# Kernel optimization log

Measured on AMD Instinct MI355X. Metric: run time of the kernel, lower is better.

Reference implementation:

```python
import jax, jax.numpy as jnp
import numpy as np

B, C, G, K, S, P, R = 4, 256, 16, 7, 1, 3, 4
H = W = 56


def setup_inputs() -> dict:
    key = jax.random.key(0)
    k1, k2, k3 = jax.random.split(key, 3)
    x = jax.random.normal(k1, (B, C, H, W), jnp.float32)
    reduce_w = jax.random.normal(k2, (C // R, C), jnp.float32) * 0.05
    reduce_b = jnp.zeros((C // R,), jnp.float32)
    span_w = jax.random.normal(k3, (K * K * G, C // R), jnp.float32) * 0.05
    span_b = jnp.zeros((K * K * G,), jnp.float32)
    return {"x": x, "reduce_w": reduce_w, "reduce_b": reduce_b,
            "span_w": span_w, "span_b": span_b}


def reference(x, reduce_w, reduce_b, span_w, span_b):
    b, c, h_in, w_in = x.shape
    Ho = (h_in + 2 * P - K) // S + 1
    Wo = (w_in + 2 * P - K) // S + 1
    # im2col patches, channel ordering (C, kh, kw) — matches torch.nn.Unfold
    patches = jax.lax.conv_general_dilated_patches(
        x, (K, K), (S, S), [(P, P), (P, P)])  # (B, C*K*K, Ho, Wo)
    patches = patches.reshape(b, G, c // G, K * K, Ho, Wo)
    # kernel generation branch: AvgPool(s) (identity for s=1) -> 1x1 reduce -> 1x1 span
    if S > 1:
        xk = jax.lax.reduce_window(x, 0.0, jax.lax.add,
                                   (1, 1, S, S), (1, 1, S, S), 'VALID') / (S * S)
    else:
        xk = x
    h = jnp.einsum('bchw,oc->bohw', xk, reduce_w) + reduce_b[None, :, None, None]
    kern = jnp.einsum('bchw,oc->bohw', h, span_w) + span_b[None, :, None, None]
    kern = kern.reshape(b, G, 1, K * K, Ho, Wo)
    # dynamic per-pixel depthwise-style multiply-reduce over the K*K window
    out = (kern * patches).sum(axis=3)  # (B, G, C//G, Ho, Wo)
    return out.reshape(b, c, Ho, Wo)
```

## Files before the change

### kernel.cpp

```cpp
#include <hip/hip_runtime.h>
#include <stdint.h>

#define HH   56
#define WW   56
#define HWP  (HH * WW)
#define CC   256
#define GG   16
#define CGR  16
#define KT   7
#define KK   49
#define RCP  32
#define TH   2
#define XP   548
#define RP   68
#define TP   116

typedef _Float16 h2_t __attribute__((ext_vector_type(2)));
typedef _Float16 v8h  __attribute__((ext_vector_type(8)));
typedef float    v4f  __attribute__((ext_vector_type(4)));
union pk32 { uint32_t u; h2_t h; };
union frag { uint32_t u[4]; v8h h; };

__global__ __launch_bounds__(256)
void pack_weights(const float* __restrict__ sw, const float* __restrict__ rw,
                  uint32_t* __restrict__ sw2, uint32_t* __restrict__ rw2)
{
    const int id = blockIdx.x * 256 + threadIdx.x;
    if (id < 25088) {
        pk32 p; p.h = h2_t{(_Float16)sw[2 * id], (_Float16)sw[2 * id + 1]};
        sw2[id] = p.u;
    } else {
        const int j = id - 25088;
        pk32 p; p.h = h2_t{(_Float16)rw[2 * j], (_Float16)rw[2 * j + 1]};
        rw2[j] = p.u;
    }
}

__global__ __launch_bounds__(256)
void gemm1_mfma(const uint32_t* __restrict__ rw2, const float* __restrict__ rb,
                const float* __restrict__ x, uint32_t* __restrict__ h2)
{
    const int b   = blockIdx.z;
    const int px0 = blockIdx.x * 32;
    const int t = threadIdx.x;
    const int wave = t >> 6, lane = t & 63, quad = lane >> 4, n16 = lane & 15;

    __shared__ __align__(16) uint32_t ldsB[2][32][36];

    const int c2l = t >> 3;
    const int px4 = t & 7;
    const float* xb = x + (size_t)b * CC * HWP + px0 + 4 * px4;

    v4f acc[2];
    acc[0] = v4f{0.f,0.f,0.f,0.f}; acc[1] = v4f{0.f,0.f,0.f,0.f};

    {
        const int c = 2 * c2l;
        const float4 a  = *(const float4*)&xb[(size_t)c * HWP];
        const float4 bb = *(const float4*)&xb[(size_t)(c + 1) * HWP];
        pk32 u0,u1,u2,u3;
        u0.h = h2_t{(_Float16)a.x, (_Float16)bb.x};
        u1.h = h2_t{(_Float16)a.y, (_Float16)bb.y};
        u2.h = h2_t{(_Float16)a.z, (_Float16)bb.z};
        u3.h = h2_t{(_Float16)a.w, (_Float16)bb.w};
        uint4 w; w.x=u0.u; w.y=u1.u; w.z=u2.u; w.w=u3.u;
        *(uint4*)&ldsB[0][c2l][4 * px4] = w;
    }
    __syncthreads();

    const uint32_t* rwm = rw2 + (size_t)(wave * 16 + n16) * 128;
#pragma unroll
    for (int k = 0; k < 4; ++k) {
        if (k < 3) {
            const int c = (k + 1) * 64 + 2 * c2l;
            const float4 a  = *(const float4*)&xb[(size_t)c * HWP];
            const float4 bb = *(const float4*)&xb[(size_t)(c + 1) * HWP];
            pk32 u0,u1,u2,u3;
            u0.h = h2_t{(_Float16)a.x, (_Float16)bb.x};
            u1.h = h2_t{(_Float16)a.y, (_Float16)bb.y};
            u2.h = h2_t{(_Float16)a.z, (_Float16)bb.z};
            u3.h = h2_t{(_Float16)a.w, (_Float16)bb.w};
            uint4 w; w.x=u0.u; w.y=u1.u; w.z=u2.u; w.w=u3.u;
            *(uint4*)&ldsB[(k + 1) & 1][c2l][4 * px4] = w;
        }
        frag a0, a1;
        *(uint4*)a0.u = *(const uint4*)&rwm[k * 32 + quad * 4];
        *(uint4*)a1.u = *(const uint4*)&rwm[k * 32 + 16 + quad * 4];
        const uint32_t (*B)[36] = ldsB[k & 1];
#pragma unroll
        for (int nt = 0; nt < 2; ++nt) {
            frag b0, b1;
#pragma unroll
            for (int jj = 0; jj < 4; ++jj) {
                b0.u[jj] = B[quad * 4 + jj][nt * 16 + n16];
                b1.u[jj] = B[16 + quad * 4 + jj][nt * 16 + n16];
            }
            acc[nt] = __builtin_amdgcn_mfma_f32_16x16x32_f16(a0.h, b0.h, acc[nt], 0, 0, 0);
            acc[nt] = __builtin_amdgcn_mfma_f32_16x16x32_f16(a1.h, b1.h, acc[nt], 0, 0, 0);
        }
        __syncthreads();
    }
    uint32_t* hb = h2 + (size_t)b * RCP * HWP + px0;
#pragma unroll
    for (int nt = 0; nt < 2; ++nt) {
#pragma unroll
        for (int pr = 0; pr < 2; ++pr) {
            const int m0 = wave * 16 + quad * 4 + 2 * pr;
            pk32 q;
            q.h = h2_t{(_Float16)(acc[nt][2 * pr] + rb[m0]),
                       (_Float16)(acc[nt][2 * pr + 1] + rb[m0 + 1])};
            hb[(size_t)(wave * 8 + quad * 2 + pr) * HWP + nt * 16 + n16] = q.u;
        }
    }
}

__global__ __launch_bounds__(256, 2)
void invol_fused(const float* __restrict__ x, const uint32_t* __restrict__ h2,
                 const uint32_t* __restrict__ sw2, const float* __restrict__ sb,
                 float* __restrict__ out)
{
    const int h0 = blockIdx.x * TH;
    const int g  = blockIdx.y;
    const int b  = blockIdx.z;

    __shared__ __align__(16) float    sX[16 * XP];
    __shared__ __align__(16) uint32_t ldsT[32 * TP];
    __shared__ __align__(16) float    sK[KK * 112];
    const int t = threadIdx.x;
    const int wave = t >> 6, lane = t & 63, quad = lane >> 4, n16 = lane & 15;

    const int mt0 = wave * 16 + n16;
    const int mtap = mt0 > 48 ? 48 : mt0;
    const uint32_t* swr = sw2 + ((size_t)g * KK + mtap) * RCP + quad * 4;
    frag a0, a1;
    *(uint4*)a0.u = *(const uint4*)swr;
    *(uint4*)a1.u = *(const uint4*)(swr + 16);

    float bvv[4];
#pragma unroll
    for (int reg = 0; reg < 4; ++reg) {
        const int tp = wave * 16 + quad * 4 + reg;
        bvv[reg] = (tp < KK) ? sb[g * KK + tp] : 0.f;
    }

    {
        const uint32_t* hb = h2 + (size_t)b * RCP * HWP + h0 * WW;
#pragma unroll
        for (int k = 0; k < 14; ++k) {
            const int i = t + 256 * k;
            const int px = i % 112, c2 = i / 112;
            ldsT[c2 * TP + px] = hb[(size_t)c2 * HWP + px];
        }
    }

    {
        const int hc = t & 1, rr = (t >> 1) & 7, ch = t >> 4;
        *(float4*)&sX[ch * XP + rr * RP + (hc ? 60 : 0)] = make_float4(0,0,0,0);
    }

    {
        const float* xb = x + (size_t)(b * CC + g * CGR) * HWP;
#pragma unroll
        for (int k = 0; k < 7; ++k) {
            const int i = t + 256 * k;
            const int w4 = i % 14, rr = (i / 14) % 8, ch = i / 112;
            const int hh = h0 - 3 + rr;
            float4 v = make_float4(0,0,0,0);
            if (hh >= 0 && hh < HH)
                v = *(const float4*)&xb[(size_t)ch * HWP + hh * WW + 4 * w4];
            *(float4*)&sX[ch * XP + rr * RP + 4 + 4 * w4] = v;
        }
    }
    __syncthreads();

    v4f acc[7];
#pragma unroll
    for (int nt = 0; nt < 7; ++nt) acc[nt] = v4f{0.f,0.f,0.f,0.f};
#pragma unroll
    for (int nt = 0; nt < 7; ++nt) {
        const int px = nt * 16 + n16;
        frag b0, b1;
#pragma unroll
        for (int jj = 0; jj < 4; ++jj) {
            b0.u[jj] = ldsT[(quad * 4 + jj) * TP + px];
            b1.u[jj] = ldsT[(16 + quad * 4 + jj) * TP + px];
        }
        acc[nt] = __builtin_amdgcn_mfma_f32_16x16x32_f16(a0.h, b0.h, acc[nt], 0, 0, 0);
        acc[nt] = __builtin_amdgcn_mfma_f32_16x16x32_f16(a1.h, b1.h, acc[nt], 0, 0, 0);
    }
#pragma unroll
    for (int nt = 0; nt < 7; ++nt) {
        const int px = nt * 16 + n16;
#pragma unroll
        for (int reg = 0; reg < 4; ++reg) {
            const int tp = wave * 16 + quad * 4 + reg;
            if (tp < KK) sK[tp * 112 + px] = acc[nt][reg] + bvv[reg];
        }
    }
    __syncthreads();

    if (t < 224) {
        const int ch = t & 15;
        const int q  = t >> 4;
        const int r  = q & 1;
        const int wq = q >> 1;
        const float* xc = sX + ch * XP;
        float* op = out + (size_t)(b * CC + g * CGR + ch) * HWP + (h0 + r) * WW;
#pragma unroll
        for (int wb = 0; wb < 2; ++wb) {
            const int w0 = 4 * wq + 28 * wb;
            float o0=0.f, o1=0.f, o2=0.f, o3=0.f;
#pragma unroll
            for (int kh = 0; kh < KT; ++kh) {
                const int rr = r + kh;
                const float* xr = xc + rr * RP + w0;
                float xf[12];
                *(float4*)&xf[0] = *(const float4*)&xr[0];
                *(float4*)&xf[4] = *(const float4*)&xr[4];
                *(float4*)&xf[8] = *(const float4*)&xr[8];
                const float* kp = sK + (kh * KT) * 112 + r * WW + w0;
#pragma unroll
                for (int kw = 0; kw < KT; ++kw) {
                    const float4 kf = *(const float4*)&kp[kw * 112];
                    o0 += kf.x * xf[kw + 1];
                    o1 += kf.y * xf[kw + 2];
                    o2 += kf.z * xf[kw + 3];
                    o3 += kf.w * xf[kw + 4];
                }
            }
            *(float4*)&op[w0] = make_float4(o0, o1, o2, o3);
        }
    }
}

extern "C" void kernel_launch(void* const* d_in, const int* in_sizes, int n_in,
                              void* d_out, int out_size, void* d_ws, size_t ws_size,
                              hipStream_t stream)
{
    const float* x  = (const float*)d_in[0];
    const float* rw = (const float*)d_in[1];
    const float* rb = (const float*)d_in[2];
    const float* sw = (const float*)d_in[3];
    const float* sb = (const float*)d_in[4];
    float* out  = (float*)d_out;

    uint32_t* h2  = (uint32_t*)d_ws;
    uint32_t* sw2 = h2 + 4 * RCP * HWP;
    uint32_t* rw2 = sw2 + 25088;

    pack_weights<<<dim3(130, 1, 1), 256, 0, stream>>>(sw, rw, sw2, rw2);
    gemm1_mfma<<<dim3(HWP / 32, 1, 4), 256, 0, stream>>>(rw2, rb, x, h2);
    invol_fused<<<dim3(HH / TH, GG, 4), 256, 0, stream>>>(x, h2, sw2, sb, out);
}
```

Before: 109.9 us.

## Convert involution inner loop to packed fp16 FMA with half-precision LDS tiles

Stores the x tile and the generated per-pixel kernels in LDS as fp16 instead of fp32, and computes the 7x7 multiply-reduce with packed __hfma2 ops, accumulating each kernel row in fp16 before adding it to fp32 totals. LDS buffers are reused and shrunk, and launch bounds are raised to allow more resident blocks per CU. The h2 tile and gemm1 B operand are rearranged so MFMA fragments load as single 128-bit reads, and all fp32-to-fp16 conversions use pkrtz. The main cost targeted is LDS footprint, LDS traffic and FMA count in the main loop; the risk is lower accuracy from fp16 partial sums and round-toward-zero conversion.

Result: faster. 96.14 us (-12.5%).

```diff
diff --git a/kernel.cpp b/kernel.cpp
--- a/kernel.cpp
+++ b/kernel.cpp
@@ -1,9 +1,10 @@
 #include <hip/hip_runtime.h>
+#include <hip/hip_fp16.h>
 #include <stdint.h>
 
 #define HH   56
 #define WW   56
-#define HWP  (HH * WW)
+#define HWP  3136
 #define CC   256
 #define GG   16
 #define CGR  16
@@ -11,90 +12,78 @@
 #define KK   49
 #define RCP  32
 #define TH   2
-#define XP   548
-#define RP   68
-#define TP   116
-
-typedef _Float16 h2_t __attribute__((ext_vector_type(2)));
+#define XROW 32
+#define XPL  260
+
+typedef _Float16 h2_t  __attribute__((ext_vector_type(2)));
+typedef __fp16   fp16x2 __attribute__((ext_vector_type(2)));
 typedef _Float16 v8h  __attribute__((ext_vector_type(8)));
 typedef float    v4f  __attribute__((ext_vector_type(4)));
-union pk32 { uint32_t u; h2_t h; };
+union pk32 { uint32_t u; h2_t h; __half2 hh; fp16x2 f; };
 union frag { uint32_t u[4]; v8h h; };
+
+static __device__ __forceinline__ uint32_t pkrtz(float a, float b) {
+    pk32 p; p.f = __builtin_amdgcn_cvt_pkrtz(a, b); return p.u;
+}
 
 __global__ __launch_bounds__(256)
 void pack_weights(const float* __restrict__ sw, const float* __restrict__ rw,
                   uint32_t* __restrict__ sw2, uint32_t* __restrict__ rw2)
 {
     const int id = blockIdx.x * 256 + threadIdx.x;
-    if (id < 25088) {
-        pk32 p; p.h = h2_t{(_Float16)sw[2 * id], (_Float16)sw[2 * id + 1]};
-        sw2[id] = p.u;
-    } else {
-        const int j = id - 25088;
-        pk32 p; p.h = h2_t{(_Float16)rw[2 * j], (_Float16)rw[2 * j + 1]};
-        rw2[j] = p.u;
-    }
+    if (id < 25088) sw2[id] = pkrtz(sw[2 * id], sw[2 * id + 1]);
+    else            rw2[id - 25088] = pkrtz(rw[2 * (id - 25088)], rw[2 * (id - 25088) + 1]);
 }
 
 __global__ __launch_bounds__(256)
 void gemm1_mfma(const uint32_t* __restrict__ rw2, const float* __restrict__ rb,
                 const float* __restrict__ x, uint32_t* __restrict__ h2)
 {
-    const int b   = blockIdx.z;
-    const int px0 = blockIdx.x * 32;
+    const int b = blockIdx.z, px0 = blockIdx.x * 32;
     const int t = threadIdx.x;
     const int wave = t >> 6, lane = t & 63, quad = lane >> 4, n16 = lane & 15;
 
-    __shared__ __align__(16) uint32_t ldsB[2][32][36];
-
-    const int c2l = t >> 3;
-    const int px4 = t & 7;
-    const float* xb = x + (size_t)b * CC * HWP + px0 + 4 * px4;
+    __shared__ __align__(16) uint32_t ldsB[2][8 * 128];
+
+    const int px = t & 31;
+    const int q4 = t >> 5;
+    const float* xb = x + (size_t)b * CC * HWP + px0 + px;
+
+    float r[4][8];
+#pragma unroll
+    for (int k = 0; k < 4; ++k)
+#pragma unroll
+        for (int cc = 0; cc < 8; ++cc)
+            r[k][cc] = xb[(size_t)(k * 64 + q4 * 8 + cc) * HWP];
+
+    {
+        uint4 w;
+        w.x = pkrtz(r[0][0], r[0][1]); w.y = pkrtz(r[0][2], r[0][3]);
+        w.z = pkrtz(r[0][4], r[0][5]); w.w = pkrtz(r[0][6], r[0][7]);
+        *(uint4*)&ldsB[0][q4 * 128 + px * 4] = w;
+    }
+    __syncthreads();
 
     v4f acc[2];
     acc[0] = v4f{0.f,0.f,0.f,0.f}; acc[1] = v4f{0.f,0.f,0.f,0.f};
-
-    {
-        const int c = 2 * c2l;
-        const float4 a  = *(const float4*)&xb[(size_t)c * HWP];
-        const float4 bb = *(const float4*)&xb[(size_t)(c + 1) * HWP];
-        pk32 u0,u1,u2,u3;
-        u0.h = h2_t{(_Float16)a.x, (_Float16)bb.x};
-        u1.h = h2_t{(_Float16)a.y, (_Float16)bb.y};
-        u2.h = h2_t{(_Float16)a.z, (_Float16)bb.z};
-        u3.h = h2_t{(_Float16)a.w, (_Float16)bb.w};
-        uint4 w; w.x=u0.u; w.y=u1.u; w.z=u2.u; w.w=u3.u;
-        *(uint4*)&ldsB[0][c2l][4 * px4] = w;
-    }
-    __syncthreads();
-
     const uint32_t* rwm = rw2 + (size_t)(wave * 16 + n16) * 128;
 #pragma unroll
     for (int k = 0; k < 4; ++k) {
         if (k < 3) {
-            const int c = (k + 1) * 64 + 2 * c2l;
-            const float4 a  = *(const float4*)&xb[(size_t)c * HWP];
-            const float4 bb = *(const float4*)&xb[(size_t)(c + 1) * HWP];
-            pk32 u0,u1,u2,u3;
-            u0.h = h2_t{(_Float16)a.x, (_Float16)bb.x};
-            u1.h = h2_t{(_Float16)a.y, (_Float16)bb.y};
-            u2.h = h2_t{(_Float16)a.z, (_Float16)bb.z};
-            u3.h = h2_t{(_Float16)a.w, (_Float16)bb.w};
-            uint4 w; w.x=u0.u; w.y=u1.u; w.z=u2.u; w.w=u3.u;
-            *(uint4*)&ldsB[(k + 1) & 1][c2l][4 * px4] = w;
+            uint4 w;
+            w.x = pkrtz(r[k+1][0], r[k+1][1]); w.y = pkrtz(r[k+1][2], r[k+1][3]);
+            w.z = pkrtz(r[k+1][4], r[k+1][5]); w.w = pkrtz(r[k+1][6], r[k+1][7]);
+            *(uint4*)&ldsB[(k + 1) & 1][q4 * 128 + px * 4] = w;
         }
         frag a0, a1;
         *(uint4*)a0.u = *(const uint4*)&rwm[k * 32 + quad * 4];
         *(uint4*)a1.u = *(const uint4*)&rwm[k * 32 + 16 + quad * 4];
-        const uint32_t (*B)[36] = ldsB[k & 1];
+        const uint32_t* B = ldsB[k & 1];
 #pragma unroll
         for (int nt = 0; nt < 2; ++nt) {
             frag b0, b1;
-#pragma unroll
-            for (int jj = 0; jj < 4; ++jj) {
-                b0.u[jj] = B[quad * 4 + jj][nt * 16 + n16];
-                b1.u[jj] = B[16 + quad * 4 + jj][nt * 16 + n16];
-            }
+            *(uint4*)b0.u = *(const uint4*)&B[quad * 128 + (nt * 16 + n16) * 4];
+            *(uint4*)b1.u = *(const uint4*)&B[(4 + quad) * 128 + (nt * 16 + n16) * 4];
             acc[nt] = __builtin_amdgcn_mfma_f32_16x16x32_f16(a0.h, b0.h, acc[nt], 0, 0, 0);
             acc[nt] = __builtin_amdgcn_mfma_f32_16x16x32_f16(a1.h, b1.h, acc[nt], 0, 0, 0);
         }
@@ -102,30 +91,25 @@
     }
     uint32_t* hb = h2 + (size_t)b * RCP * HWP + px0;
 #pragma unroll
-    for (int nt = 0; nt < 2; ++nt) {
+    for (int nt = 0; nt < 2; ++nt)
 #pragma unroll
         for (int pr = 0; pr < 2; ++pr) {
             const int m0 = wave * 16 + quad * 4 + 2 * pr;
-            pk32 q;
-            q.h = h2_t{(_Float16)(acc[nt][2 * pr] + rb[m0]),
-                       (_Float16)(acc[nt][2 * pr + 1] + rb[m0 + 1])};
-            hb[(size_t)(wave * 8 + quad * 2 + pr) * HWP + nt * 16 + n16] = q.u;
-        }
-    }
-}
-
-__global__ __launch_bounds__(256, 2)
+            hb[(size_t)(wave * 8 + quad * 2 + pr) * HWP + nt * 16 + n16] =
+                pkrtz(acc[nt][2 * pr] + rb[m0], acc[nt][2 * pr + 1] + rb[m0 + 1]);
+        }
+}
+
+__global__ __launch_bounds__(256, 4)
 void invol_fused(const float* __restrict__ x, const uint32_t* __restrict__ h2,
                  const uint32_t* __restrict__ sw2, const float* __restrict__ sb,
                  float* __restrict__ out)
 {
-    const int h0 = blockIdx.x * TH;
-    const int g  = blockIdx.y;
-    const int b  = blockIdx.z;
-
-    __shared__ __align__(16) float    sX[16 * XP];
-    __shared__ __align__(16) uint32_t ldsT[32 * TP];
-    __shared__ __align__(16) float    sK[KK * 112];
+    const int h0 = blockIdx.x * TH, g = blockIdx.y, b = blockIdx.z;
+
+    __shared__ __align__(16) uint32_t sXh[16 * XPL];
+    __shared__ __align__(16) uint32_t U[8 * 448];
+
     const int t = threadIdx.x;
     const int wave = t >> 6, lane = t & 63, quad = lane >> 4, n16 = lane & 15;
 
@@ -146,16 +130,24 @@
     {
         const uint32_t* hb = h2 + (size_t)b * RCP * HWP + h0 * WW;
 #pragma unroll
-        for (int k = 0; k < 14; ++k) {
+        for (int k = 0; k < 4; ++k) {
             const int i = t + 256 * k;
-            const int px = i % 112, c2 = i / 112;
-            ldsT[c2 * TP + px] = hb[(size_t)c2 * HWP + px];
-        }
-    }
-
-    {
-        const int hc = t & 1, rr = (t >> 1) & 7, ch = t >> 4;
-        *(float4*)&sX[ch * XP + rr * RP + (hc ? 60 : 0)] = make_float4(0,0,0,0);
+            if (i < 896) {
+                const int px = i % 112, q4 = i / 112;
+                uint4 w;
+                w.x = hb[(size_t)(q4 * 4 + 0) * HWP + px];
+                w.y = hb[(size_t)(q4 * 4 + 1) * HWP + px];
+                w.z = hb[(size_t)(q4 * 4 + 2) * HWP + px];
+                w.w = hb[(size_t)(q4 * 4 + 3) * HWP + px];
+                *(uint4*)&U[q4 * 448 + px * 4] = w;
+            }
+        }
+    }
+
+    {
+        const int ch = t >> 4, rr = (t >> 1) & 7, side = t & 1;
+        uint2 z; z.x = 0; z.y = 0;
+        *(uint2*)&sXh[ch * XPL + rr * XROW + (side ? 30 : 0)] = z;
     }
 
     {
@@ -165,10 +157,11 @@
             const int i = t + 256 * k;
             const int w4 = i % 14, rr = (i / 14) % 8, ch = i / 112;
             const int hh = h0 - 3 + rr;
-            float4 v = make_float4(0,0,0,0);
+            float4 v = make_float4(0.f, 0.f, 0.f, 0.f);
             if (hh >= 0 && hh < HH)
                 v = *(const float4*)&xb[(size_t)ch * HWP + hh * WW + 4 * w4];
-            *(float4*)&sX[ch * XP + rr * RP + 4 + 4 * w4] = v;
+            uint2 p; p.x = pkrtz(v.x, v.y); p.y = pkrtz(v.z, v.w);
+            *(uint2*)&sXh[ch * XPL + rr * XROW + 2 + 2 * w4] = p;
         }
     }
     __syncthreads();
@@ -178,58 +171,70 @@
     for (int nt = 0; nt < 7; ++nt) acc[nt] = v4f{0.f,0.f,0.f,0.f};
 #pragma unroll
     for (int nt = 0; nt < 7; ++nt) {
-        const int px = nt * 16 + n16;
+        const int pxm = (nt * 16 + n16) * 4;
         frag b0, b1;
-#pragma unroll
-        for (int jj = 0; jj < 4; ++jj) {
-            b0.u[jj] = ldsT[(quad * 4 + jj) * TP + px];
-            b1.u[jj] = ldsT[(16 + quad * 4 + jj) * TP + px];
-        }
+        *(uint4*)b0.u = *(const uint4*)&U[quad * 448 + pxm];
+        *(uint4*)b1.u = *(const uint4*)&U[(4 + quad) * 448 + pxm];
         acc[nt] = __builtin_amdgcn_mfma_f32_16x16x32_f16(a0.h, b0.h, acc[nt], 0, 0, 0);
         acc[nt] = __builtin_amdgcn_mfma_f32_16x16x32_f16(a1.h, b1.h, acc[nt], 0, 0, 0);
     }
-#pragma unroll
-    for (int nt = 0; nt < 7; ++nt) {
-        const int px = nt * 16 + n16;
-#pragma unroll
-        for (int reg = 0; reg < 4; ++reg) {
-            const int tp = wave * 16 + quad * 4 + reg;
-            if (tp < KK) sK[tp * 112 + px] = acc[nt][reg] + bvv[reg];
+    __syncthreads();
+
+    {
+        _Float16* sK = (_Float16*)U;
+#pragma unroll
+        for (int nt = 0; nt < 7; ++nt) {
+            const int px = nt * 16 + n16;
+#pragma unroll
+            for (int reg = 0; reg < 4; ++reg) {
+                const int tp = wave * 16 + quad * 4 + reg;
+                if (tp < KK) sK[tp * 112 + px] = (_Float16)(acc[nt][reg] + bvv[reg]);
+            }
         }
     }
     __syncthreads();
 
     if (t < 224) {
-        const int ch = t & 15;
-        const int q  = t >> 4;
-        const int r  = q & 1;
-        const int wq = q >> 1;
-        const float* xc = sX + ch * XP;
-        float* op = out + (size_t)(b * CC + g * CGR + ch) * HWP + (h0 + r) * WW;
-#pragma unroll
-        for (int wb = 0; wb < 2; ++wb) {
-            const int w0 = 4 * wq + 28 * wb;
-            float o0=0.f, o1=0.f, o2=0.f, o3=0.f;
-#pragma unroll
-            for (int kh = 0; kh < KT; ++kh) {
-                const int rr = r + kh;
-                const float* xr = xc + rr * RP + w0;
-                float xf[12];
-                *(float4*)&xf[0] = *(const float4*)&xr[0];
-                *(float4*)&xf[4] = *(const float4*)&xr[4];
-                *(float4*)&xf[8] = *(const float4*)&xr[8];
-                const float* kp = sK + (kh * KT) * 112 + r * WW + w0;
-#pragma unroll
-                for (int kw = 0; kw < KT; ++kw) {
-                    const float4 kf = *(const float4*)&kp[kw * 112];
-                    o0 += kf.x * xf[kw + 1];
-                    o1 += kf.y * xf[kw + 2];
-                    o2 += kf.z * xf[kw + 3];
-                    o3 += kf.w * xf[kw + 4];
+        const int ch = t & 15, q = t >> 4, r = q & 1, wq = q >> 1;
+        const uint32_t* xpl = &sXh[ch * XPL + 4 * wq];
+        float o0=0,o1=0,o2=0,o3=0,o4=0,o5=0,o6=0,o7=0;
+#pragma unroll
+        for (int kh = 0; kh < KT; ++kh) {
+            const int rr = r + kh;
+            uint32_t E[8];
+            *(uint4*)&E[0] = *(const uint4*)&xpl[rr * XROW];
+            *(uint4*)&E[4] = *(const uint4*)&xpl[rr * XROW + 4];
+            uint32_t O[7];
+#pragma unroll
+            for (int j = 0; j < 7; ++j) O[j] = __builtin_amdgcn_alignbit(E[j + 1], E[j], 16);
+            pk32 va0, va1, va2, va3;
+            va0.u = va1.u = va2.u = va3.u = 0;
+            const uint32_t* kq = &U[(kh * KT) * 56 + r * 28 + 4 * wq];
+#pragma unroll
+            for (int kw = 0; kw < KT; ++kw) {
+                const uint4 kk = *(const uint4*)&kq[kw * 56];
+                pk32 k0, k1, k2, k3; k0.u = kk.x; k1.u = kk.y; k2.u = kk.z; k3.u = kk.w;
+                pk32 s0, s1, s2, s3;
+                if (kw & 1) {
+                    const int e = (kw + 1) >> 1;
+                    s0.u = E[e]; s1.u = E[e + 1]; s2.u = E[e + 2]; s3.u = E[e + 3];
+                } else {
+                    const int oI = kw >> 1;
+                    s0.u = O[oI]; s1.u = O[oI + 1]; s2.u = O[oI + 2]; s3.u = O[oI + 3];
                 }
+                va0.hh = __hfma2(k0.hh, s0.hh, va0.hh);
+                va1.hh = __hfma2(k1.hh, s1.hh, va1.hh);
+                va2.hh = __hfma2(k2.hh, s2.hh, va2.hh);
+                va3.hh = __hfma2(k3.hh, s3.hh, va3.hh);
             }
-            *(float4*)&op[w0] = make_float4(o0, o1, o2, o3);
-        }
+            const float2 f0 = __half22float2(va0.hh); o0 += f0.x; o1 += f0.y;
+            const float2 f1 = __half22float2(va1.hh); o2 += f1.x; o3 += f1.y;
+            const float2 f2 = __half22float2(va2.hh); o4 += f2.x; o5 += f2.y;
+            const float2 f3 = __half22float2(va3.hh); o6 += f3.x; o7 += f3.y;
+        }
+        float* op = out + (size_t)(b * CC + g * CGR + ch) * HWP + (h0 + r) * WW + 8 * wq;
+        *(float4*)&op[0] = make_float4(o0, o1, o2, o3);
+        *(float4*)&op[4] = make_float4(o4, o5, o6, o7);
     }
 }
 
```
